# Kernel optimization log

Measured on AMD Instinct MI355X. Metric: run time of the kernel, lower is better.

Reference implementation:

```python
import jax, jax.numpy as jnp
import numpy as np

# module config (init_kwargs)
AH, AW = 14, 14            # aligned_height, aligned_width
SCALE = 0.25               # spatial_scale
RATIO = 2                  # sampling_ratio
SHIFT = 0.0                # spatial_shift (added in feature-map coords)
HALF_PART = 0              # 0 = full box
ROI_SCALE = 1.0            # box rescale about its center


def setup_inputs() -> dict:
    key = jax.random.key(0)
    kf, kb, kx, ky, kw, kh = jax.random.split(key, 6)
    B, C, H, W = 2, 256, 200, 272
    N = 256
    features = jax.random.normal(kf, (B, C, H, W), dtype=jnp.float32)
    img_h, img_w = H / SCALE, W / SCALE
    bidx = jax.random.randint(kb, (N,), 0, B).astype(jnp.float32)
    x1 = jax.random.uniform(kx, (N,)) * (img_w * 0.6)
    y1 = jax.random.uniform(ky, (N,)) * (img_h * 0.6)
    bw = 32.0 + jax.random.uniform(kw, (N,)) * (img_w * 0.35)
    bh = 32.0 + jax.random.uniform(kh, (N,)) * (img_h * 0.35)
    rois = jnp.stack([bidx, x1, y1, x1 + bw, y1 + bh], axis=1).astype(jnp.float32)
    return {"features": features, "rois": rois}


def _lin_idx(coord, size):
    # bilinear index/weight prep with RoIAlign boundary rules
    valid = (coord > -1.0) & (coord < float(size))
    c = jnp.clip(coord, 0.0, float(size - 1))
    lo = jnp.floor(c)
    hi = jnp.minimum(lo + 1.0, float(size - 1))
    frac = c - lo
    return lo.astype(jnp.int32), hi.astype(jnp.int32), frac, valid.astype(coord.dtype)


def _roi_mask_align(features, rois):
    B, C, H, W = features.shape
    N = rois.shape[0]
    PH, PW, r = AH + 1, AW + 1, RATIO
    b = rois[:, 0].astype(jnp.int32)
    # to feature-map coords, with roi_scale about the box center and spatial_shift
    x1, y1, x2, y2 = (rois[:, 1] * SCALE, rois[:, 2] * SCALE,
                      rois[:, 3] * SCALE, rois[:, 4] * SCALE)
    cx, cy = 0.5 * (x1 + x2), 0.5 * (y1 + y2)
    hw, hh = 0.5 * (x2 - x1) * ROI_SCALE, 0.5 * (y2 - y1) * ROI_SCALE
    x1, x2 = cx - hw + SHIFT, cx + hw + SHIFT
    y1, y2 = cy - hh + SHIFT, cy + hh + SHIFT
    roi_w = jnp.maximum(x2 - x1, 1.0)
    roi_h = jnp.maximum(y2 - y1, 1.0)
    bin_w = roi_w / PW
    bin_h = roi_h / PH
    # sample coords, separable: sx [N, PW*r], sy [N, PH*r]
    ix = jnp.arange(PW * r, dtype=jnp.float32)
    iy = jnp.arange(PH * r, dtype=jnp.float32)
    sx = x1[:, None] + (ix[None, :] + 0.5) * (bin_w[:, None] / r)
    sy = y1[:, None] + (iy[None, :] + 0.5) * (bin_h[:, None] / r)
    y_lo, y_hi, fy, vy = _lin_idx(sy, H)
    x_lo, x_hi, fx, vx = _lin_idx(sx, W)
    featsT = jnp.transpose(features, (0, 2, 3, 1))  # [B,H,W,C]
    bb = b[:, None, None]
    gather = lambda yi, xi: featsT[bb, yi[:, :, None], xi[:, None, :]]  # [N,Sy,Sx,C]
    wy0, wy1 = 1.0 - fy, fy
    wx0, wx1 = 1.0 - fx, fx
    val = (gather(y_lo, x_lo) * (wy0[:, :, None] * wx0[:, None, :])[..., None]
           + gather(y_lo, x_hi) * (wy0[:, :, None] * wx1[:, None, :])[..., None]
           + gather(y_hi, x_lo) * (wy1[:, :, None] * wx0[:, None, :])[..., None]
           + gather(y_hi, x_hi) * (wy1[:, :, None] * wx1[:, None, :])[..., None])
    val = val * (vy[:, :, None] * vx[:, None, :])[..., None]
    # average the r*r samples per bin -> [N, PH, PW, C]
    val = val.reshape(N, PH, r, PW, r, C).mean(axis=(2, 4))
    return jnp.transpose(val, (0, 3, 1, 2))  # [N, C, PH, PW]


def reference(features, rois):
    x = _roi_mask_align(features, rois)  # [N, C, AH+1, AW+1]
    # avg_pool2d(kernel=2, stride=1)
    out = 0.25 * (x[..., :-1, :-1] + x[..., 1:, :-1]
                  + x[..., :-1, 1:] + x[..., 1:, 1:])
    return out  # [N, C, AH, AW]
```

## Files before the change

kernel.cpp:

```cpp
#include <hip/hip_runtime.h>


#define AH_ 14
#define AW_ 14
#define NS_ 30
#define C_  256
#define H_  200
#define W_  272
#define CPB 4
#define VS_ 33
#define HS_ 15

__global__ __launch_bounds__(256)
void roi_mask_align_avg_kernel(const float* __restrict__ feat,
                               const float* __restrict__ rois,
                               float* __restrict__ out) {
    __shared__ float V[CPB][NS_ * VS_];
    __shared__ float Hs[CPB][NS_ * HS_];

    const int p   = blockIdx.x;
    const int xcd = p & 7;
    const int q   = p >> 3;
    const int n   = q & 255;
    const int cgi = q >> 8;
    const int cg  = cgi * 8 + xcd;
    const int c0  = cg * CPB;

    const int tid  = threadIdx.x;
    const int wave = tid >> 6;
    const int lane = tid & 63;
    const int ix   = lane & 31;
    const int half = lane >> 5;

    const float r0f = rois[n * 5 + 0];
    const float x1s = rois[n * 5 + 1] * 0.25f;
    const float y1s = rois[n * 5 + 2] * 0.25f;
    const float x2s = rois[n * 5 + 3] * 0.25f;
    const float y2s = rois[n * 5 + 4] * 0.25f;
    const int   b   = (int)r0f;

    const float cx = 0.5f * (x1s + x2s), cy = 0.5f * (y1s + y2s);
    const float hw = 0.5f * (x2s - x1s), hh = 0.5f * (y2s - y1s);
    const float x1 = cx - hw, x2 = cx + hw;
    const float y1 = cy - hh, y2 = cy + hh;
    const float roi_w = fmaxf(x2 - x1, 1.0f);
    const float roi_h = fmaxf(y2 - y1, 1.0f);
    const float sub_w = roi_w * (1.0f / 15.0f) * 0.5f;
    const float sub_h = roi_h * (1.0f / 15.0f) * 0.5f;

    const float sx  = x1 + ((float)ix + 0.5f) * sub_w;
    const bool  vx_ = (sx > -1.0f) && (sx < (float)W_);
    const float ccx = fminf(fmaxf(sx, 0.0f), (float)(W_ - 1));
    const float lox = floorf(ccx);
    const int   xl  = (int)lox;
    const int   xh  = min(xl + 1, W_ - 1);
    const float fx  = ccx - lox;
    const float vmx = vx_ ? 1.0f : 0.0f;
    const float wx0 = (1.0f - fx) * vmx;
    const float wx1 = fx * vmx;

    const int c = c0 + wave;
    const float* __restrict__ fp = feat + ((size_t)b * C_ + c) * (size_t)(H_ * W_);
    float* __restrict__ Vw = V[wave];

    #pragma unroll 5
    for (int ps = 0; ps < 15; ++ps) {
        const int   iy  = 2 * ps + half;
        const float sy  = y1 + ((float)iy + 0.5f) * sub_h;
        const bool  vy_ = (sy > -1.0f) && (sy < (float)H_);
        const float ccy = fminf(fmaxf(sy, 0.0f), (float)(H_ - 1));
        const float loy = floorf(ccy);
        const int   yl  = (int)loy;
        const int   yh  = min(yl + 1, H_ - 1);
        const float fy  = ccy - loy;
        const float vmy = vy_ ? 1.0f : 0.0f;
        const float wy0 = (1.0f - fy) * vmy;
        const float wy1 = fy * vmy;

        const float* r0p = fp + yl * W_;
        const float* r1p = fp + yh * W_;
        const float v = r0p[xl] * (wy0 * wx0) + r0p[xh] * (wy0 * wx1)
                      + r1p[xl] * (wy1 * wx0) + r1p[xh] * (wy1 * wx1);
        if (ix < NS_) Vw[iy * VS_ + ix] = v;
    }
    __syncthreads();

    float* __restrict__ Hw = Hs[wave];
    for (int o = lane; o < NS_ * AW_; o += 64) {
        const int iy = o / AW_;
        const int aw = o - iy * AW_;
        const float* vr = Vw + iy * VS_ + 2 * aw;
        Hw[iy * HS_ + aw] = vr[0] + vr[1] + vr[2] + vr[3];
    }
    __syncthreads();

    float* __restrict__ op = out + ((size_t)n * C_ + c) * (AH_ * AW_);
    for (int o = lane; o < AH_ * AW_; o += 64) {
        const int ah = o / AW_;
        const int aw = o - ah * AW_;
        const float* hr = Hw + (2 * ah) * HS_ + aw;
        op[o] = (hr[0] + hr[HS_] + hr[2 * HS_] + hr[3 * HS_]) * (1.0f / 16.0f);
    }
}

extern "C" void kernel_launch(void* const* d_in, const int* in_sizes, int n_in,
                              void* d_out, int out_size, void* d_ws, size_t ws_size,
                              hipStream_t stream) {
    const float* feat = (const float*)d_in[0];
    const float* rois = (const float*)d_in[1];
    float* out = (float*)d_out;
    const int grid = 256 * (C_ / CPB);
    roi_mask_align_avg_kernel<<<grid, 256, 0, stream>>>(feat, rois, out);
}
```

Before: 254.5 us.

## Replace LDS pooling stages with wave shuffles and process four channels per wave

Drops the two shared-memory staging buffers and both block barriers. The 2x2 horizontal sum and the cross-half vertical sum are now done with cross-lane shuffles, and the previous bin row is kept in registers so each output row is written directly. Each wave now handles four channels instead of one, giving more independent gathers in flight, and the grid shrinks by the same factor. The 1/16 averaging is folded into the bilinear weights. The cost is more register pressure and fewer, longer-running blocks.

Measured after the change: 303.3 us. 19.2% more time.

```diff
diff --git a/kernel.cpp b/kernel.cpp
--- a/kernel.cpp
+++ b/kernel.cpp
@@ -1,22 +1,21 @@
 #include <hip/hip_runtime.h>
 
 
-#define AH_ 14
-#define AW_ 14
-#define NS_ 30
 #define C_  256
 #define H_  200
 #define W_  272
-#define CPB 4
-#define VS_ 33
-#define HS_ 15
+#define CPW 4
+#define CPB (CPW * 4)
 
 __global__ __launch_bounds__(256)
 void roi_mask_align_avg_kernel(const float* __restrict__ feat,
                                const float* __restrict__ rois,
                                float* __restrict__ out) {
-    __shared__ float V[CPB][NS_ * VS_];
-    __shared__ float Hs[CPB][NS_ * HS_];
+    const int tid  = threadIdx.x;
+    const int wave = tid >> 6;
+    const int lane = tid & 63;
+    const int ix   = lane & 31;
+    const int half = lane >> 5;
 
     const int p   = blockIdx.x;
     const int xcd = p & 7;
@@ -24,13 +23,7 @@
     const int n   = q & 255;
     const int cgi = q >> 8;
     const int cg  = cgi * 8 + xcd;
-    const int c0  = cg * CPB;
-
-    const int tid  = threadIdx.x;
-    const int wave = tid >> 6;
-    const int lane = tid & 63;
-    const int ix   = lane & 31;
-    const int half = lane >> 5;
+    const int c0  = cg * CPB + wave * CPW;
 
     const float r0f = rois[n * 5 + 0];
     const float x1s = rois[n * 5 + 1] * 0.25f;
@@ -49,57 +42,56 @@
     const float sub_h = roi_h * (1.0f / 15.0f) * 0.5f;
 
     const float sx  = x1 + ((float)ix + 0.5f) * sub_w;
-    const bool  vx_ = (sx > -1.0f) && (sx < (float)W_);
+    const float vmx = ((sx > -1.0f) && (sx < (float)W_)) ? 0.25f : 0.0f;
     const float ccx = fminf(fmaxf(sx, 0.0f), (float)(W_ - 1));
     const float lox = floorf(ccx);
     const int   xl  = (int)lox;
     const int   xh  = min(xl + 1, W_ - 1);
-    const float fx  = ccx - lox;
-    const float vmx = vx_ ? 1.0f : 0.0f;
-    const float wx0 = (1.0f - fx) * vmx;
-    const float wx1 = fx * vmx;
+    const float fxv = ccx - lox;
+    const float wx0 = (1.0f - fxv) * vmx;
+    const float wx1 = fxv * vmx;
 
-    const int c = c0 + wave;
-    const float* __restrict__ fp = feat + ((size_t)b * C_ + c) * (size_t)(H_ * W_);
-    float* __restrict__ Vw = V[wave];
+    const size_t HW = (size_t)H_ * W_;
+    const float* __restrict__ fp0 = feat + ((size_t)b * C_ + c0) * HW;
+    float* __restrict__ op0 = out + ((size_t)n * C_ + c0) * 196;
 
-    #pragma unroll 5
+    const bool writer = (half == 0) && ((ix & 1) == 0) && (ix < 28);
+    const int  ocol   = ix >> 1;
+
+    float prev[CPW];
+    #pragma unroll
+    for (int k = 0; k < CPW; ++k) prev[k] = 0.0f;
+
     for (int ps = 0; ps < 15; ++ps) {
         const int   iy  = 2 * ps + half;
         const float sy  = y1 + ((float)iy + 0.5f) * sub_h;
-        const bool  vy_ = (sy > -1.0f) && (sy < (float)H_);
+        const float vmy = ((sy > -1.0f) && (sy < (float)H_)) ? 0.25f : 0.0f;
         const float ccy = fminf(fmaxf(sy, 0.0f), (float)(H_ - 1));
         const float loy = floorf(ccy);
         const int   yl  = (int)loy;
         const int   yh  = min(yl + 1, H_ - 1);
-        const float fy  = ccy - loy;
-        const float vmy = vy_ ? 1.0f : 0.0f;
-        const float wy0 = (1.0f - fy) * vmy;
-        const float wy1 = fy * vmy;
+        const float fyv = ccy - loy;
+        const float wy0 = (1.0f - fyv) * vmy;
+        const float wy1 = fyv * vmy;
 
-        const float* r0p = fp + yl * W_;
-        const float* r1p = fp + yh * W_;
-        const float v = r0p[xl] * (wy0 * wx0) + r0p[xh] * (wy0 * wx1)
-                      + r1p[xl] * (wy1 * wx0) + r1p[xh] * (wy1 * wx1);
-        if (ix < NS_) Vw[iy * VS_ + ix] = v;
-    }
-    __syncthreads();
+        const float w00 = wy0 * wx0, w01 = wy0 * wx1;
+        const float w10 = wy1 * wx0, w11 = wy1 * wx1;
+        const int o00 = yl * W_ + xl, o01 = yl * W_ + xh;
+        const int o10 = yh * W_ + xl, o11 = yh * W_ + xh;
 
-    float* __restrict__ Hw = Hs[wave];
-    for (int o = lane; o < NS_ * AW_; o += 64) {
-        const int iy = o / AW_;
-        const int aw = o - iy * AW_;
-        const float* vr = Vw + iy * VS_ + 2 * aw;
-        Hw[iy * HS_ + aw] = vr[0] + vr[1] + vr[2] + vr[3];
-    }
-    __syncthreads();
-
-    float* __restrict__ op = out + ((size_t)n * C_ + c) * (AH_ * AW_);
-    for (int o = lane; o < AH_ * AW_; o += 64) {
-        const int ah = o / AW_;
-        const int aw = o - ah * AW_;
-        const float* hr = Hw + (2 * ah) * HS_ + aw;
-        op[o] = (hr[0] + hr[HS_] + hr[2 * HS_] + hr[3 * HS_]) * (1.0f / 16.0f);
+        #pragma unroll
+        for (int k = 0; k < CPW; ++k) {
+            const float* __restrict__ fpk = fp0 + (size_t)k * HW;
+            const float v = fpk[o00] * w00 + fpk[o01] * w01
+                          + fpk[o10] * w10 + fpk[o11] * w11;
+            const float s1 = v  + __shfl_xor(v, 1);
+            const float hs = s1 + __shfl_down(s1, 2);
+            const float pr = hs + __shfl_xor(hs, 32);
+            if (ps > 0 && writer) {
+                op0[(size_t)k * 196 + (ps - 1) * 14 + ocol] = prev[k] + pr;
+            }
+            prev[k] = pr;
+        }
     }
 }
 
```
